# Optimization experiments

Measured on AMD Instinct MI355X. Metric: run time of the kernel, lower is better.

## Reference

```python
import jax, jax.numpy as jnp
import numpy as np

H = 4        # num_heads
KNN = 10     # k_knn neighbors gathered by distance
KS = 4       # k_select top-k neighbors kept by attention score
EPS = 1e-5
BIG = 1e9


def _ln(x, g, b):
    m = x.mean(-1, keepdims=True)
    v = ((x - m) ** 2).mean(-1, keepdims=True)
    return (x - m) * jax.lax.rsqrt(v + EPS) * g + b


def _sparse_dyn_voxel_attn(x, coords, mask, w_qkv, b_qkv, w_proj, b_proj):
    # x: [B,N,C], coords: [B,N,3], mask: [B,N] bool
    B, N, C = x.shape
    dh = C // H
    qkv = x @ w_qkv + b_qkv                       # [B,N,3C]
    q, k, v = jnp.split(qkv, 3, axis=-1)
    q = q.reshape(B, N, H, dh).transpose(0, 2, 1, 3)   # [B,H,N,dh]
    k = k.reshape(B, N, H, dh).transpose(0, 2, 1, 3)
    v = v.reshape(B, N, H, dh).transpose(0, 2, 1, 3)

    # KNN over voxel coordinates; empty voxels pushed to far distance
    d2 = jnp.sum((coords[:, :, None, :] - coords[:, None, :, :]) ** 2, axis=-1)  # [B,N,N]
    d2 = jnp.where(mask[:, None, :], d2, BIG)
    _, nbr = jax.lax.top_k(-d2, KNN)              # [B,N,KNN] nearest-neighbor indices

    # gather neighbor keys/values: [B,H,N,KNN,dh]
    kn = jax.vmap(lambda a, i: a[:, i, :])(k, nbr)
    vn = jax.vmap(lambda a, i: a[:, i, :])(v, nbr)
    nmask = jax.vmap(lambda m, i: m[i])(mask, nbr)  # [B,N,KNN]

    scale = float(1.0 / np.sqrt(dh))
    scores = jnp.einsum('bhnd,bhnkd->bhnk', q, kn) * scale  # [B,H,N,KNN]
    scores = scores + jnp.where(nmask, 0.0, -BIG)[:, None, :, :]

    # dynamic selection: keep top k_select neighbors by score, softmax over them
    sv, si = jax.lax.top_k(scores, KS)            # [B,H,N,KS]
    w = jax.nn.softmax(sv, axis=-1)
    vsel = jnp.take_along_axis(vn, si[..., None], axis=3)   # [B,H,N,KS,dh]
    o = jnp.einsum('bhnk,bhnkd->bhnd', w, vsel)   # [B,H,N,dh]
    o = o.transpose(0, 2, 1, 3).reshape(B, N, C) @ w_proj + b_proj
    return jnp.where(mask[..., None], o, 0.0)


def setup_inputs() -> dict:
    key = jax.random.key(0)
    ks = jax.random.split(key, 8)
    B, N, C, M = 4, 4096, 64, 256  # N = 16^3 voxels
    s = lambda k, sh: jax.random.normal(k, sh, jnp.float32) * 0.02
    return dict(
        inputs=jax.random.normal(ks[0], (B, N, C), jnp.float32),
        voxel_coords=jax.random.uniform(ks[1], (B, N, 3), jnp.float32) * 16.0,
        non_empty_mask=jax.random.randint(ks[2], (B, N), 0, 2).astype(bool),
        ln1_g=jnp.ones(C, jnp.float32), ln1_b=jnp.zeros(C, jnp.float32),
        ln2_g=jnp.ones(C, jnp.float32), ln2_b=jnp.zeros(C, jnp.float32),
        w_qkv=s(ks[3], (C, 3 * C)), b_qkv=jnp.zeros(3 * C, jnp.float32),
        w_proj=s(ks[4], (C, C)), b_proj=jnp.zeros(C, jnp.float32),
        w1=s(ks[5], (C, M)), b1=jnp.zeros(M, jnp.float32),
        w2=s(ks[6], (M, C)), b2=jnp.zeros(C, jnp.float32),
    )


def reference(inputs, voxel_coords, non_empty_mask, ln1_g, ln1_b, ln2_g, ln2_b,
              w_qkv, b_qkv, w_proj, b_proj, w1, b1, w2, b2):
    a = _sparse_dyn_voxel_attn(_ln(inputs, ln1_g, ln1_b), voxel_coords,
                               non_empty_mask, w_qkv, b_qkv, w_proj, b_proj)
    x = 0.5 * a + inputs                          # drop_path(attn)*0.5 + shortcut (eval)
    h = jax.nn.gelu(_ln(x, ln2_g, ln2_b) @ w1 + b1) @ w2 + b2
    return 0.5 * h + x
```

## Files before the change

### kernel.cpp

```cpp
#include <hip/hip_runtime.h>
#include <hip/hip_bf16.h>
#include <math.h>

#define NH   4
#define DH   16
#define CH   64
#define KNN  10
#define KS   4
#define NV   4096
#define NB   4
#define MHID 256
#define BN   (NB * NV)

#define P_LN1G  0
#define P_LN1B  64
#define P_LN2G  128
#define P_LN2B  192
#define P_WQKV  256
#define P_BQKV  12544
#define P_WPROJ 12736
#define P_BPROJ 16832
#define P_W1    16896
#define P_B1    33280
#define P_W2    33536
#define P_B2    49920
#define P_TOT   49984

#define N_ING  (BN * CH + NB * NV * 3 + P_TOT + BN)
#define N_PACK (16384 + 16384 + 12288)

typedef __hip_bfloat16 bf16;
typedef __attribute__((ext_vector_type(8))) short short8;
typedef __attribute__((ext_vector_type(4))) float float4a;

__device__ __forceinline__ float b2f(bf16 x) { return __bfloat162float(x); }

__device__ __forceinline__ float cvt(const void* p, int i, int isbf) {
  return isbf ? b2f(((const bf16*)p)[i]) : ((const float*)p)[i];
}

__device__ __forceinline__ float wave_sum_f32(float v) {
#pragma unroll
  for (int m = 32; m >= 1; m >>= 1) v += __shfl_xor(v, m, 64);
  return v;
}

__device__ __forceinline__ void wave_min_kv(unsigned& hi, unsigned& lo) {
#pragma unroll
  for (int m = 32; m >= 1; m >>= 1) {
    unsigned ohi = __shfl_xor(hi, m, 64);
    unsigned olo = __shfl_xor(lo, m, 64);
    if (ohi < hi || (ohi == hi && olo < lo)) { hi = ohi; lo = olo; }
  }
}

__device__ __forceinline__ float tanh_fast(float u) {
  float e = __expf(2.0f * u);
  return 1.0f - 2.0f / (e + 1.0f);
}

__device__ __forceinline__ float d2f(float x, float y, float z,
                                     float qx, float qy, float qz) {
  float dx = x - qx, dy = y - qy, dz = z - qz;
  return dx * dx + dy * dy + dz * dz;
}

__global__ __launch_bounds__(256) void k_prep(
    const void* xin, const void* coords, const void* maskr,
    const void* ln1g, const void* ln1b, const void* ln2g, const void* ln2b,
    const void* wqkv, const void* bqkv, const void* wproj, const void* bproj,
    const void* w1, const void* b1, const void* w2, const void* b2,
    float* __restrict__ xcan, float* __restrict__ ccan,
    float* __restrict__ pcan, int* __restrict__ mcan,
    unsigned short* __restrict__ w1p, unsigned short* __restrict__ w2p,
    unsigned short* __restrict__ wqp, int* __restrict__ flags)
{
  __shared__ int sfl[2];
  const int tid = threadIdx.x;
  if (tid < 64) {
    const unsigned short* xu = (const unsigned short*)xin;
    const unsigned* mu = (const unsigned*)maskr;
    int cnt = 0;
#pragma unroll
    for (int k = 0; k < 4; ++k) {
      unsigned short w = xu[tid * 4 + k];
      int e = (w >> 7) & 0xFF;
      cnt += (e >= 100 && e <= 140);
    }
#pragma unroll
    for (int m = 32; m >= 1; m >>= 1) cnt += __shfl_xor(cnt, m, 64);
    unsigned big = (mu[tid] > 1u) ? 1u : 0u;
#pragma unroll
    for (int m = 32; m >= 1; m >>= 1) big |= __shfl_xor(big, m, 64);
    if (tid == 0) {
      sfl[0] = (cnt >= 205) ? 1 : 0;
      sfl[1] = big ? 1 : 0;
      if (blockIdx.x == 0) { flags[0] = sfl[0]; flags[1] = sfl[1]; }
    }
  }
  __syncthreads();
  const int isbf = sfl[0], m8 = sfl[1];

  int id = blockIdx.x * 256 + tid;
  const int n0 = BN * CH, n1 = NB * NV * 3, n2 = P_TOT, n3 = BN;
  if (id < n0) { xcan[id] = cvt(xin, id, isbf); return; }
  id -= n0;
  if (id < n1) { ccan[id] = cvt(coords, id, isbf); return; }
  id -= n1;
  if (id < n2) {
    const void* src; int off;
    if      (id < P_LN1B)  { src = ln1g;  off = id - P_LN1G; }
    else if (id < P_LN2G)  { src = ln1b;  off = id - P_LN1B; }
    else if (id < P_LN2B)  { src = ln2g;  off = id - P_LN2G; }
    else if (id < P_WQKV)  { src = ln2b;  off = id - P_LN2B; }
    else if (id < P_BQKV)  { src = wqkv;  off = id - P_WQKV; }
    else if (id < P_WPROJ) { src = bqkv;  off = id - P_BQKV; }
    else if (id < P_BPROJ) { src = wproj; off = id - P_WPROJ; }
    else if (id < P_W1)    { src = bproj; off = id - P_BPROJ; }
    else if (id < P_B1)    { src = w1;    off = id - P_W1; }
    else if (id < P_W2)    { src = b1;    off = id - P_B1; }
    else if (id < P_B2)    { src = w2;    off = id - P_W2; }
    else                   { src = b2;    off = id - P_B2; }
    pcan[id] = cvt(src, off, isbf);
    return;
  }
  id -= n2;
  if (id < n3) {
    mcan[id] = m8 ? (int)(((const unsigned char*)maskr)[id] != 0)
                  : (int)(((const int*)maskr)[id] != 0);
    return;
  }
  id -= n3;
  if (id < 16384) {
    int j = id & 7, l = (id >> 3) & 63, kh = (id >> 9) & 1, nt = id >> 10;
    int k = kh * 32 + ((l >> 4) * 8) + j;
    int n = nt * 16 + (l & 15);
    w1p[id] = __bfloat16_as_ushort(__float2bfloat16(cvt(w1, k * MHID + n, isbf)));
    return;
  }
  id -= 16384;
  if (id < 16384) {
    int j = id & 7, l = (id >> 3) & 63, kh = (id >> 9) & 7, nt = id >> 12;
    int k = kh * 32 + ((l >> 4) * 8) + j;
    int n = nt * 16 + (l & 15);
    w2p[id] = __bfloat16_as_ushort(__float2bfloat16(cvt(w2, k * CH + n, isbf)));
    return;
  }
  id -= 16384;
  if (id < 12288) {
    int j = id & 7, l = (id >> 3) & 63, kh = (id >> 9) & 1, nt = id >> 10;
    int k = kh * 32 + ((l >> 4) * 8) + j;
    int n = nt * 16 + (l & 15);
    wqp[id] = __bfloat16_as_ushort(__float2bfloat16(cvt(wqkv, k * 192 + n, isbf)));
  }
}

#define XQS 72
__global__ __launch_bounds__(256) void k_ln_qkv(
    const float* __restrict__ x, const float* __restrict__ pcan,
    const unsigned short* __restrict__ wqp, float* __restrict__ qkv)
{
  __shared__ unsigned short xnb[16 * XQS];
  const int tid = threadIdx.x;
  const int wave = tid >> 6, lane = tid & 63;
  const int row0 = blockIdx.x * 16;

  {
    const float gg = pcan[P_LN1G + lane], bb = pcan[P_LN1B + lane];
#pragma unroll
    for (int r = 0; r < 4; ++r) {
      int m = wave * 4 + r;
      float v = x[(size_t)(row0 + m) * CH + lane];
      float mn = wave_sum_f32(v) * (1.0f / 64.0f);
      float d = v - mn;
      float var = wave_sum_f32(d * d) * (1.0f / 64.0f);
      float rs = 1.0f / sqrtf(var + 1e-5f);
      xnb[m * XQS + lane] =
          __bfloat16_as_ushort(__float2bfloat16(d * rs * gg + bb));
    }
  }
  __syncthreads();

  const int q = lane >> 4, c = lane & 15;
  short8 a0 = *(const short8*)&xnb[c * XQS + q * 8];
  short8 a1 = *(const short8*)&xnb[c * XQS + 32 + q * 8];

#pragma unroll
  for (int t = 0; t < 3; ++t) {
    int nt = wave * 3 + t;
    short8 b0 = *(const short8*)&wqp[(size_t)((nt * 2 + 0) * 64 + lane) * 8];
    short8 b1 = *(const short8*)&wqp[(size_t)((nt * 2 + 1) * 64 + lane) * 8];
    float4a z = {0.f, 0.f, 0.f, 0.f};
    z = __builtin_amdgcn_mfma_f32_16x16x32_bf16(a0, b0, z, 0, 0, 0);
    z = __builtin_amdgcn_mfma_f32_16x16x32_bf16(a1, b1, z, 0, 0, 0);
    int n = nt * 16 + c;
    float bq = pcan[P_BQKV + n];
#pragma unroll
    for (int r = 0; r < 4; ++r) {
      int m = q * 4 + r;
      qkv[(size_t)(row0 + m) * 192 + n] = z[r] + bq;
    }
  }
}

#define KROWS 4
#define CAP   128
__global__ __launch_bounds__(256) void k_knn(
    const float* __restrict__ ccan, const int* __restrict__ mcan,
    int* __restrict__ nbr)
{
  __shared__ float4 sx[NV / 4], sy[NV / 4], sz[NV / 4];
  __shared__ unsigned long long sbuf[KROWS][CAP];
  const int tid = threadIdx.x;
  const int row0 = blockIdx.x * KROWS;
  const int b = row0 >> 12;
  const float* cb = ccan + (size_t)b * NV * 3;
  const int* mb = mcan + b * NV;

  float* fx = (float*)sx; float* fy = (float*)sy; float* fz = (float*)sz;
  for (int j = tid; j < NV; j += 256) {
    bool v = mb[j] != 0;
    float x = cb[j * 3], y = cb[j * 3 + 1], z = cb[j * 3 + 2];
    fx[j] = v ? x : 1e4f;
    fy[j] = v ? y : 1e4f;
    fz[j] = v ? z : 1e4f;
  }
  __syncthreads();
  const int wave = tid >> 6, lane = tid & 63;
  const int qi = (row0 & (NV - 1)) + wave;
  const float qx = cb[qi * 3], qy = cb[qi * 3 + 1], qz = cb[qi * 3 + 2];

  float bmin = 1e30f;
#pragma unroll 4
  for (int t = 0; t < 16; ++t) {
    float4 X = sx[lane + t * 64], Y = sy[lane + t * 64], Z = sz[lane + t * 64];
    float d0 = d2f(X.x, Y.x, Z.x, qx, qy, qz);
    float d1 = d2f(X.y, Y.y, Z.y, qx, qy, qz);
    float d2 = d2f(X.z, Y.z, Z.z, qx, qy, qz);
    float d3 = d2f(X.w, Y.w, Z.w, qx, qy, qz);
    bmin = fminf(bmin, fminf(fminf(d0, d1), fminf(d2, d3)));
  }

  const unsigned lm = __float_as_uint(bmin);
  unsigned acc = 0;
#pragma unroll 1
  for (int bit = 31; bit >= 0; --bit) {
    unsigned tr = acc | (1u << bit);
    int cnt = __popcll(__ballot(lm < tr));
    if (cnt <= KNN - 1) acc = tr;
  }
  const float T = __uint_as_float(acc + 8);

  int base = 0;
  const unsigned long long below = (lane == 0) ? 0ull : (~0ull >> (64 - lane));
#pragma unroll 4
  for (int t = 0; t < 16; ++t) {
    float4 X = sx[lane + t * 64], Y = sy[lane + t * 64], Z = sz[lane + t * 64];
    float dd[4];
    dd[0] = d2f(X.x, Y.x, Z.x, qx, qy, qz);
    dd[1] = d2f(X.y, Y.y, Z.y, qx, qy, qz);
    dd[2] = d2f(X.z, Y.z, Z.z, qx, qy, qz);
    dd[3] = d2f(X.w, Y.w, Z.w, qx, qy, qz);
#pragma unroll
    for (int e = 0; e < 4; ++e) {
      bool s = (dd[e] <= T);
      unsigned long long bal = __ballot(s);
      if (bal) {
        int pos = base + __popcll(bal & below);
        unsigned j = 4u * (unsigned)(lane + t * 64) + (unsigned)e;
        if (s && pos < CAP)
          sbuf[wave][pos] =
              ((unsigned long long)__float_as_uint(dd[e]) << 32) | j;
        base += __popcll(bal);
      }
    }
  }
  const int c = base;
  const int grow = row0 + wave;

  if (c >= KNN && c <= CAP) {
#pragma unroll
    for (int o = 0; o < 2; ++o) {
      int idx = lane + o * 64;
      if (idx < c) {
        unsigned long long mykey = sbuf[wave][idx];
        int rank = 0;
        for (int i = 0; i < c; ++i) rank += (sbuf[wave][i] < mykey);
        if (rank < KNN)
          nbr[(size_t)grow * KNN + rank] = (int)(mykey & (NV - 1));
      }
    }
  } else {
    unsigned long long arr[KNN];
#pragma unroll
    for (int t = 0; t < KNN; ++t) arr[t] = ~0ull;
    for (int t = 0; t < 16; ++t) {
      float4 X = sx[lane + t * 64], Y = sy[lane + t * 64], Z = sz[lane + t * 64];
      float dd[4];
      dd[0] = d2f(X.x, Y.x, Z.x, qx, qy, qz);
      dd[1] = d2f(X.y, Y.y, Z.y, qx, qy, qz);
      dd[2] = d2f(X.z, Y.z, Z.z, qx, qy, qz);
      dd[3] = d2f(X.w, Y.w, Z.w, qx, qy, qz);
#pragma unroll
      for (int e = 0; e < 4; ++e) {
        unsigned j = 4u * (unsigned)(lane + t * 64) + (unsigned)e;
        unsigned long long key =
            ((unsigned long long)__float_as_uint(dd[e]) << 32) | j;
        if (key < arr[KNN - 1]) {
          arr[KNN - 1] = key;
#pragma unroll
          for (int t2 = KNN - 1; t2 > 0; --t2) {
            unsigned long long a = arr[t2 - 1], cc = arr[t2];
            if (cc < a) { arr[t2 - 1] = cc; arr[t2] = a; }
          }
        }
      }
    }
    unsigned myj = 0;
#pragma unroll 1
    for (int r = 0; r < KNN; ++r) {
      unsigned hi = (unsigned)(arr[0] >> 32);
      unsigned lo = (unsigned)(arr[0] & 0xffffffffu);
      wave_min_kv(hi, lo);
      if (lane == (int)((lo >> 2) & 63u)) {
#pragma unroll
        for (int t = 0; t < KNN - 1; ++t) arr[t] = arr[t + 1];
        arr[KNN - 1] = ~0ull;
      }
      if (lane == r) myj = lo;
    }
    if (lane < KNN) nbr[(size_t)grow * KNN + lane] = (int)(myj & (NV - 1));
  }
}

#define AROWS 4
__global__ __launch_bounds__(256) void k_attn(
    const float* __restrict__ qkv, const int* __restrict__ nbr,
    const int* __restrict__ mcan, const float* __restrict__ xcan,
    const float* __restrict__ pcan, float* __restrict__ xres)
{
  __shared__ float wp[CH * CH];
  __shared__ float bp[CH];
  __shared__ float sc[AROWS][NH][KNN];
  __shared__ float wsel[AROWS][NH][KS];
  __shared__ int   isel[AROWS][NH][KS];
  __shared__ float obuf[AROWS][CH];
  __shared__ int   nb[AROWS][KNN];
  __shared__ float npen[AROWS][KNN];
  const int tid = threadIdx.x;
  {
    const float4* src = (const float4*)(pcan + P_WPROJ);
    float4* dst = (float4*)wp;
    for (int i = tid; i < CH * CH / 4; i += 256) dst[i] = src[i];
    if (tid < CH) bp[tid] = pcan[P_BPROJ + tid];
  }
  const int wave = tid >> 6, lane = tid & 63;
  const int row = blockIdx.x * AROWS + wave;
  const int b = row / NV;

  if (lane < KNN) {
    int j = nbr[(size_t)row * KNN + lane] & (NV - 1);
    nb[wave][lane] = j;
    npen[wave][lane] = mcan[b * NV + j] ? 0.0f : -1e9f;
  }
  __syncthreads();

  if (lane < NH * KNN) {
    int h = lane / KNN, kk = lane % KNN;
    int j = nb[wave][kk];
    const float* qp = qkv + (size_t)row * 192 + h * DH;
    const float* kp = qkv + ((size_t)(b * NV + j)) * 192 + 64 + h * DH;
    float acc = 0.f;
#pragma unroll
    for (int d = 0; d < DH; ++d) acc += qp[d] * kp[d];
    sc[wave][h][kk] = acc * 0.25f + npen[wave][kk];
  }
  __syncthreads();

  if (lane < NH) {
    int h = lane;
    float sv[KS]; int sj[KS];
    unsigned used = 0;
#pragma unroll
    for (int r = 0; r < KS; ++r) {
      float best = -INFINITY; int bi = 0;
#pragma unroll
      for (int kk = 0; kk < KNN; ++kk) {
        float s = sc[wave][h][kk];
        if (!(used & (1u << kk)) && s > best) { best = s; bi = kk; }
      }
      used |= 1u << bi; sv[r] = best; sj[r] = bi;
    }
    float mx = sv[0];
    float e[KS], sum = 0.f;
#pragma unroll
    for (int r = 0; r < KS; ++r) { e[r] = expf(sv[r] - mx); sum += e[r]; }
    float inv = 1.0f / sum;
#pragma unroll
    for (int r = 0; r < KS; ++r) {
      wsel[wave][h][r] = e[r] * inv;
      isel[wave][h][r] = nb[wave][sj[r]];
    }
  }
  __syncthreads();

  {
    int h = lane >> 4, d = lane & 15;
    float o = 0.f;
#pragma unroll
    for (int r = 0; r < KS; ++r) {
      int j = isel[wave][h][r];
      o += wsel[wave][h][r] * qkv[((size_t)(b * NV + j)) * 192 + 128 + h * DH + d];
    }
    obuf[wave][lane] = o;
  }
  __syncthreads();

  {
    float acc = bp[lane];
#pragma unroll 4
    for (int cc = 0; cc < CH; ++cc)
      acc = fmaf(obuf[wave][cc], wp[cc * CH + lane], acc);
    float a = mcan[row] ? acc : 0.0f;
    xres[(size_t)row * CH + lane] = 0.5f * a + xcan[(size_t)row * CH + lane];
  }
}

#define XNS 72
#define GS  264
__global__ __launch_bounds__(256) void k_mlp(
    const float* __restrict__ xres, const float* __restrict__ pcan,
    const unsigned short* __restrict__ w1p,
    const unsigned short* __restrict__ w2p,
    const int* __restrict__ flags, void* __restrict__ out)
{
  __shared__ unsigned short xnb[16 * XNS];
  __shared__ unsigned short gb[16 * GS];
  const int tid = threadIdx.x;
  const int wave = tid >> 6, lane = tid & 63;
  const int row0 = blockIdx.x * 16;

  {
    const float gg = pcan[P_LN2G + lane], bb2 = pcan[P_LN2B + lane];
#pragma unroll
    for (int r = 0; r < 4; ++r) {
      int m = wave * 4 + r;
      float v = xres[(size_t)(row0 + m) * CH + lane];
      float mn = wave_sum_f32(v) * (1.0f / 64.0f);
      float d = v - mn;
      float var = wave_sum_f32(d * d) * (1.0f / 64.0f);
      float rs = 1.0f / sqrtf(var + 1e-5f);
      xnb[m * XNS + lane] =
          __bfloat16_as_ushort(__float2bfloat16(d * rs * gg + bb2));
    }
  }
  __syncthreads();

  const int q = lane >> 4, c = lane & 15;
  short8 a0 = *(const short8*)&xnb[c * XNS + q * 8];
  short8 a1 = *(const short8*)&xnb[c * XNS + 32 + q * 8];

  float4a acc[4];
#pragma unroll
  for (int t = 0; t < 4; ++t) {
    int nt = wave * 4 + t;
    short8 b0 = *(const short8*)&w1p[(size_t)((nt * 2 + 0) * 64 + lane) * 8];
    short8 b1 = *(const short8*)&w1p[(size_t)((nt * 2 + 1) * 64 + lane) * 8];
    float4a z = {0.f, 0.f, 0.f, 0.f};
    z = __builtin_amdgcn_mfma_f32_16x16x32_bf16(a0, b0, z, 0, 0, 0);
    z = __builtin_amdgcn_mfma_f32_16x16x32_bf16(a1, b1, z, 0, 0, 0);
    acc[t] = z;
  }
#pragma unroll
  for (int t = 0; t < 4; ++t) {
    int n = (wave * 4 + t) * 16 + c;
    float bo = pcan[P_B1 + n];
#pragma unroll
    for (int r = 0; r < 4; ++r) {
      float h = acc[t][r] + bo;
      float u = 0.7978845608028654f * (h + 0.044715f * h * h * h);
      float gv = 0.5f * h * (1.0f + tanh_fast(u));
      gb[(q * 4 + r) * GS + n] = __bfloat16_as_ushort(__float2bfloat16(gv));
    }
  }
  __syncthreads();

  float4a o = {0.f, 0.f, 0.f, 0.f};
#pragma unroll
  for (int kh = 0; kh < 8; ++kh) {
    short8 ag = *(const short8*)&gb[c * GS + kh * 32 + q * 8];
    short8 bg = *(const short8*)&w2p[(size_t)((wave * 8 + kh) * 64 + lane) * 8];
    o = __builtin_amdgcn_mfma_f32_16x16x32_bf16(ag, bg, o, 0, 0, 0);
  }
  {
    int n = wave * 16 + c;
    float b2v = pcan[P_B2 + n];
    const int isbf = flags[0];
#pragma unroll
    for (int r = 0; r < 4; ++r) {
      int m = q * 4 + r;
      size_t idx = (size_t)(row0 + m) * CH + n;
      float val = 0.5f * (o[r] + b2v) + xres[idx];
      if (isbf) ((bf16*)out)[idx] = __float2bfloat16(val);
      else      ((float*)out)[idx] = val;
    }
  }
}

extern "C" void kernel_launch(void* const* d_in, const int* in_sizes, int n_in,
                              void* d_out, int out_size, void* d_ws, size_t ws_size,
                              hipStream_t stream)
{
  char* ws = (char*)d_ws;
  float* qkv   = (float*)(ws);
  float* xres  = (float*)(ws + 12582912);
  float* xcan  = (float*)(ws + 16777216);
  float* ccan  = (float*)(ws + 20971520);
  float* pcan  = (float*)(ws + 21168128);
  int*   mcan  = (int*)  (ws + 21368064);
  int*   nbr   = (int*)  (ws + 21433600);
  int*   flags = (int*)  (ws + 22088960);
  unsigned short* w1p = (unsigned short*)(ws + 22089728);
  unsigned short* w2p = (unsigned short*)(ws + 22122496);
  unsigned short* wqp = (unsigned short*)(ws + 22155264);

  const int total = N_ING + N_PACK;
  k_prep<<<(total + 255) / 256, 256, 0, stream>>>(
      d_in[0], d_in[1], d_in[2], d_in[3], d_in[4], d_in[5], d_in[6],
      d_in[7], d_in[8], d_in[9], d_in[10], d_in[11], d_in[12], d_in[13], d_in[14],
      xcan, ccan, pcan, mcan, w1p, w2p, wqp, flags);
  k_ln_qkv<<<BN / 16, 256, 0, stream>>>(xcan, pcan, wqp, qkv);
  k_knn<<<BN / KROWS, 256, 0, stream>>>(ccan, mcan, nbr);
  k_attn<<<BN / AROWS, 256, 0, stream>>>(qkv, nbr, mcan, xcan, pcan, xres);
  k_mlp<<<BN / 16, 256, 0, stream>>>(xres, pcan, w1p, w2p, flags, d_out);
}
```

Before: 171.5 us.

## Replace brute-force KNN with uniform-grid binning and ring search

A new kernel counting-sorts the valid voxels of each batch into a 16^3 grid of cells, with a scan producing per-cell start offsets. A per-thread KNN kernel then searches expanding rings of cells around each valid query, keeping a sorted top-10 of (distance, index) keys. It stops once the 10th distance is within the ring radius. This replaces the O(N^2) all-pairs distance scan with a mostly local search. The attention kernel also skips its work for masked rows and just copies the residual. The cost is per-thread divergence and irregular, uncoalesced loads from binned points.

```diff
diff --git a/kernel.cpp b/kernel.cpp
--- a/kernel.cpp
+++ b/kernel.cpp
@@ -45,15 +45,6 @@
   return v;
 }
 
-__device__ __forceinline__ void wave_min_kv(unsigned& hi, unsigned& lo) {
-#pragma unroll
-  for (int m = 32; m >= 1; m >>= 1) {
-    unsigned ohi = __shfl_xor(hi, m, 64);
-    unsigned olo = __shfl_xor(lo, m, 64);
-    if (ohi < hi || (ohi == hi && olo < lo)) { hi = ohi; lo = olo; }
-  }
-}
-
 __device__ __forceinline__ float tanh_fast(float u) {
   float e = __expf(2.0f * u);
   return 1.0f - 2.0f / (e + 1.0f);
@@ -63,6 +54,21 @@
                                      float qx, float qy, float qz) {
   float dx = x - qx, dy = y - qy, dz = z - qz;
   return dx * dx + dy * dy + dz * dz;
+}
+
+__device__ __forceinline__ void knn_insert(unsigned long long* arr,
+                                           unsigned long long key) {
+  if (key < arr[KNN - 1]) {
+#pragma unroll
+    for (int t = 0; t < KNN; ++t) {
+      unsigned long long a = arr[t];
+      bool lt = key < a;
+      unsigned long long mn = lt ? key : a;
+      unsigned long long mx = lt ? a : key;
+      arr[t] = mn;
+      key = mx;
+    }
+  }
 }
 
 __global__ __launch_bounds__(256) void k_prep(
@@ -203,134 +209,150 @@
   }
 }
 
-#define KROWS 4
-#define CAP   128
-__global__ __launch_bounds__(256) void k_knn(
+__global__ __launch_bounds__(1024) void k_bin(
     const float* __restrict__ ccan, const int* __restrict__ mcan,
-    int* __restrict__ nbr)
-{
-  __shared__ float4 sx[NV / 4], sy[NV / 4], sz[NV / 4];
-  __shared__ unsigned long long sbuf[KROWS][CAP];
-  const int tid = threadIdx.x;
-  const int row0 = blockIdx.x * KROWS;
-  const int b = row0 >> 12;
+    float4* __restrict__ pbin, unsigned* __restrict__ bstart)
+{
+  __shared__ unsigned cnt[NV];
+  __shared__ unsigned woff[16];
+  const int b = blockIdx.x, tid = threadIdx.x;
   const float* cb = ccan + (size_t)b * NV * 3;
   const int* mb = mcan + b * NV;
-
-  float* fx = (float*)sx; float* fy = (float*)sy; float* fz = (float*)sz;
-  for (int j = tid; j < NV; j += 256) {
-    bool v = mb[j] != 0;
-    float x = cb[j * 3], y = cb[j * 3 + 1], z = cb[j * 3 + 2];
-    fx[j] = v ? x : 1e4f;
-    fy[j] = v ? y : 1e4f;
-    fz[j] = v ? z : 1e4f;
-  }
-  __syncthreads();
-  const int wave = tid >> 6, lane = tid & 63;
-  const int qi = (row0 & (NV - 1)) + wave;
-  const float qx = cb[qi * 3], qy = cb[qi * 3 + 1], qz = cb[qi * 3 + 2];
-
-  float bmin = 1e30f;
-#pragma unroll 4
-  for (int t = 0; t < 16; ++t) {
-    float4 X = sx[lane + t * 64], Y = sy[lane + t * 64], Z = sz[lane + t * 64];
-    float d0 = d2f(X.x, Y.x, Z.x, qx, qy, qz);
-    float d1 = d2f(X.y, Y.y, Z.y, qx, qy, qz);
-    float d2 = d2f(X.z, Y.z, Z.z, qx, qy, qz);
-    float d3 = d2f(X.w, Y.w, Z.w, qx, qy, qz);
-    bmin = fminf(bmin, fminf(fminf(d0, d1), fminf(d2, d3)));
-  }
-
-  const unsigned lm = __float_as_uint(bmin);
-  unsigned acc = 0;
-#pragma unroll 1
-  for (int bit = 31; bit >= 0; --bit) {
-    unsigned tr = acc | (1u << bit);
-    int cnt = __popcll(__ballot(lm < tr));
-    if (cnt <= KNN - 1) acc = tr;
-  }
-  const float T = __uint_as_float(acc + 8);
-
-  int base = 0;
-  const unsigned long long below = (lane == 0) ? 0ull : (~0ull >> (64 - lane));
-#pragma unroll 4
-  for (int t = 0; t < 16; ++t) {
-    float4 X = sx[lane + t * 64], Y = sy[lane + t * 64], Z = sz[lane + t * 64];
-    float dd[4];
-    dd[0] = d2f(X.x, Y.x, Z.x, qx, qy, qz);
-    dd[1] = d2f(X.y, Y.y, Z.y, qx, qy, qz);
-    dd[2] = d2f(X.z, Y.z, Z.z, qx, qy, qz);
-    dd[3] = d2f(X.w, Y.w, Z.w, qx, qy, qz);
-#pragma unroll
-    for (int e = 0; e < 4; ++e) {
-      bool s = (dd[e] <= T);
-      unsigned long long bal = __ballot(s);
-      if (bal) {
-        int pos = base + __popcll(bal & below);
-        unsigned j = 4u * (unsigned)(lane + t * 64) + (unsigned)e;
-        if (s && pos < CAP)
-          sbuf[wave][pos] =
-              ((unsigned long long)__float_as_uint(dd[e]) << 32) | j;
-        base += __popcll(bal);
-      }
-    }
-  }
-  const int c = base;
-  const int grow = row0 + wave;
-
-  if (c >= KNN && c <= CAP) {
-#pragma unroll
-    for (int o = 0; o < 2; ++o) {
-      int idx = lane + o * 64;
-      if (idx < c) {
-        unsigned long long mykey = sbuf[wave][idx];
-        int rank = 0;
-        for (int i = 0; i < c; ++i) rank += (sbuf[wave][i] < mykey);
-        if (rank < KNN)
-          nbr[(size_t)grow * KNN + rank] = (int)(mykey & (NV - 1));
-      }
-    }
-  } else {
-    unsigned long long arr[KNN];
-#pragma unroll
-    for (int t = 0; t < KNN; ++t) arr[t] = ~0ull;
-    for (int t = 0; t < 16; ++t) {
-      float4 X = sx[lane + t * 64], Y = sy[lane + t * 64], Z = sz[lane + t * 64];
-      float dd[4];
-      dd[0] = d2f(X.x, Y.x, Z.x, qx, qy, qz);
-      dd[1] = d2f(X.y, Y.y, Z.y, qx, qy, qz);
-      dd[2] = d2f(X.z, Y.z, Z.z, qx, qy, qz);
-      dd[3] = d2f(X.w, Y.w, Z.w, qx, qy, qz);
-#pragma unroll
-      for (int e = 0; e < 4; ++e) {
-        unsigned j = 4u * (unsigned)(lane + t * 64) + (unsigned)e;
-        unsigned long long key =
-            ((unsigned long long)__float_as_uint(dd[e]) << 32) | j;
-        if (key < arr[KNN - 1]) {
-          arr[KNN - 1] = key;
-#pragma unroll
-          for (int t2 = KNN - 1; t2 > 0; --t2) {
-            unsigned long long a = arr[t2 - 1], cc = arr[t2];
-            if (cc < a) { arr[t2 - 1] = cc; arr[t2] = a; }
+  unsigned* st = bstart + (size_t)b * 4104;
+
+#pragma unroll
+  for (int k = 0; k < 4; ++k) cnt[tid + k * 1024] = 0;
+  __syncthreads();
+
+#pragma unroll
+  for (int k = 0; k < 4; ++k) {
+    int j = tid + k * 1024;
+    if (mb[j]) {
+      int cx = (int)cb[j * 3];     cx = cx > 15 ? 15 : cx;
+      int cy = (int)cb[j * 3 + 1]; cy = cy > 15 ? 15 : cy;
+      int cz = (int)cb[j * 3 + 2]; cz = cz > 15 ? 15 : cz;
+      atomicAdd(&cnt[(cz << 8) + (cy << 4) + cx], 1u);
+    }
+  }
+  __syncthreads();
+
+  unsigned s0 = cnt[tid * 4], s1 = cnt[tid * 4 + 1];
+  unsigned s2 = cnt[tid * 4 + 2], s3 = cnt[tid * 4 + 3];
+  unsigned tot = s0 + s1 + s2 + s3;
+  unsigned v = tot;
+  const int wv = tid >> 6, ln = tid & 63;
+#pragma unroll
+  for (int d = 1; d < 64; d <<= 1) {
+    unsigned o = __shfl_up(v, d, 64);
+    if (ln >= d) v += o;
+  }
+  if (ln == 63) woff[wv] = v;
+  __syncthreads();
+  unsigned wpre = 0;
+  for (int w = 0; w < wv; ++w) wpre += woff[w];
+  unsigned r = wpre + v - tot;
+  cnt[tid * 4]     = r; st[tid * 4]     = r; r += s0;
+  cnt[tid * 4 + 1] = r; st[tid * 4 + 1] = r; r += s1;
+  cnt[tid * 4 + 2] = r; st[tid * 4 + 2] = r; r += s2;
+  cnt[tid * 4 + 3] = r; st[tid * 4 + 3] = r; r += s3;
+  if (tid == 1023) st[4096] = r;
+  __syncthreads();
+
+#pragma unroll
+  for (int k = 0; k < 4; ++k) {
+    int j = tid + k * 1024;
+    if (mb[j]) {
+      float x = cb[j * 3], y = cb[j * 3 + 1], z = cb[j * 3 + 2];
+      int cx = (int)x; cx = cx > 15 ? 15 : cx;
+      int cy = (int)y; cy = cy > 15 ? 15 : cy;
+      int cz = (int)z; cz = cz > 15 ? 15 : cz;
+      unsigned pos = atomicAdd(&cnt[(cz << 8) + (cy << 4) + cx], 1u);
+      float4 q; q.x = x; q.y = y; q.z = z; q.w = __int_as_float(j);
+      pbin[(size_t)b * NV + pos] = q;
+    }
+  }
+}
+
+__global__ __launch_bounds__(256) void k_knn2(
+    const float4* __restrict__ pbin, const unsigned* __restrict__ bstart,
+    int* __restrict__ nbr)
+{
+  const int g = blockIdx.x * 256 + threadIdx.x;
+  const int b = g >> 12, slot = g & (NV - 1);
+  const unsigned* st = bstart + (size_t)b * 4104;
+  const int nval = (int)st[4096];
+  if (slot >= nval) return;
+  const float4* pb = pbin + (size_t)b * NV;
+  float4 me = pb[slot];
+  const float qx = me.x, qy = me.y, qz = me.z;
+  const int qi = __float_as_int(me.w);
+  int cx = (int)qx; cx = cx > 15 ? 15 : cx;
+  int cy = (int)qy; cy = cy > 15 ? 15 : cy;
+  int cz = (int)qz; cz = cz > 15 ? 15 : cz;
+
+  unsigned long long arr[KNN];
+#pragma unroll
+  for (int t = 0; t < KNN; ++t) arr[t] = ~0ull;
+
+  for (int R = 0; R < 16; ++R) {
+    const int zlo = cz - R, zhi = cz + R;
+    const int z0 = zlo < 0 ? 0 : zlo, z1 = zhi > 15 ? 15 : zhi;
+    for (int z = z0; z <= z1; ++z) {
+      const bool zed = (z == zlo) || (z == zhi);
+      const int ylo = cy - R, yhi = cy + R;
+      const int y0 = ylo < 0 ? 0 : ylo, y1 = yhi > 15 ? 15 : yhi;
+      for (int y = y0; y <= y1; ++y) {
+        const bool yed = (y == ylo) || (y == yhi);
+        const int base = (z << 8) + (y << 4);
+        if (zed || yed) {
+          const int xa = (cx - R) < 0 ? 0 : (cx - R);
+          const int xb = (cx + R) > 15 ? 15 : (cx + R);
+          const int s = (int)st[base + xa], e = (int)st[base + xb + 1];
+          for (int i = s; i < e; ++i) {
+            float4 p = pb[i];
+            float d2 = d2f(p.x, p.y, p.z, qx, qy, qz);
+            unsigned long long key =
+                ((unsigned long long)__float_as_uint(d2) << 32) |
+                (unsigned)__float_as_int(p.w);
+            knn_insert(arr, key);
+          }
+        } else {
+          const int xl = cx - R, xr = cx + R;
+          if (xl >= 0) {
+            const int s = (int)st[base + xl], e = (int)st[base + xl + 1];
+            for (int i = s; i < e; ++i) {
+              float4 p = pb[i];
+              float d2 = d2f(p.x, p.y, p.z, qx, qy, qz);
+              unsigned long long key =
+                  ((unsigned long long)__float_as_uint(d2) << 32) |
+                  (unsigned)__float_as_int(p.w);
+              knn_insert(arr, key);
+            }
+          }
+          if (xr <= 15) {
+            const int s = (int)st[base + xr], e = (int)st[base + xr + 1];
+            for (int i = s; i < e; ++i) {
+              float4 p = pb[i];
+              float d2 = d2f(p.x, p.y, p.z, qx, qy, qz);
+              unsigned long long key =
+                  ((unsigned long long)__float_as_uint(d2) << 32) |
+                  (unsigned)__float_as_int(p.w);
+              knn_insert(arr, key);
+            }
           }
         }
       }
     }
-    unsigned myj = 0;
-#pragma unroll 1
-    for (int r = 0; r < KNN; ++r) {
-      unsigned hi = (unsigned)(arr[0] >> 32);
-      unsigned lo = (unsigned)(arr[0] & 0xffffffffu);
-      wave_min_kv(hi, lo);
-      if (lane == (int)((lo >> 2) & 63u)) {
-#pragma unroll
-        for (int t = 0; t < KNN - 1; ++t) arr[t] = arr[t + 1];
-        arr[KNN - 1] = ~0ull;
-      }
-      if (lane == r) myj = lo;
-    }
-    if (lane < KNN) nbr[(size_t)grow * KNN + lane] = (int)(myj & (NV - 1));
-  }
+    if (arr[KNN - 1] != ~0ull) {
+      float dk = __uint_as_float((unsigned)(arr[KNN - 1] >> 32));
+      if (dk <= (float)(R * R)) break;
+    }
+  }
+
+  const int row = (b << 12) | qi;
+#pragma unroll
+  for (int t = 0; t < KNN; ++t)
+    nbr[(size_t)row * KNN + t] = (int)(arr[t] & (NV - 1));
 }
 
 #define AROWS 4
@@ -357,15 +379,16 @@
   const int wave = tid >> 6, lane = tid & 63;
   const int row = blockIdx.x * AROWS + wave;
   const int b = row / NV;
-
-  if (lane < KNN) {
+  const bool live = mcan[row] != 0;
+
+  if (live && lane < KNN) {
     int j = nbr[(size_t)row * KNN + lane] & (NV - 1);
     nb[wave][lane] = j;
     npen[wave][lane] = mcan[b * NV + j] ? 0.0f : -1e9f;
   }
   __syncthreads();
 
-  if (lane < NH * KNN) {
+  if (live && lane < NH * KNN) {
     int h = lane / KNN, kk = lane % KNN;
     int j = nb[wave][kk];
     const float* qp = qkv + (size_t)row * 192 + h * DH;
@@ -377,7 +400,7 @@
   }
   __syncthreads();
 
-  if (lane < NH) {
+  if (live && lane < NH) {
     int h = lane;
     float sv[KS]; int sj[KS];
     unsigned used = 0;
@@ -404,7 +427,7 @@
   }
   __syncthreads();
 
-  {
+  if (live) {
     int h = lane >> 4, d = lane & 15;
     float o = 0.f;
 #pragma unroll
@@ -416,13 +439,14 @@
   }
   __syncthreads();
 
-  {
+  if (live) {
     float acc = bp[lane];
 #pragma unroll 4
     for (int cc = 0; cc < CH; ++cc)
       acc = fmaf(obuf[wave][cc], wp[cc * CH + lane], acc);
-    float a = mcan[row] ? acc : 0.0f;
-    xres[(size_t)row * CH + lane] = 0.5f * a + xcan[(size_t)row * CH + lane];
+    xres[(size_t)row * CH + lane] = 0.5f * acc + xcan[(size_t)row * CH + lane];
+  } else {
+    xres[(size_t)row * CH + lane] = xcan[(size_t)row * CH + lane];
   }
 }
 
@@ -523,14 +547,17 @@
   unsigned short* w1p = (unsigned short*)(ws + 22089728);
   unsigned short* w2p = (unsigned short*)(ws + 22122496);
   unsigned short* wqp = (unsigned short*)(ws + 22155264);
+  float4*   pbin   = (float4*)  (ws + 22179840);
+  unsigned* bstart = (unsigned*)(ws + 22441984);
 
   const int total = N_ING + N_PACK;
   k_prep<<<(total + 255) / 256, 256, 0, stream>>>(
       d_in[0], d_in[1], d_in[2], d_in[3], d_in[4], d_in[5], d_in[6],
       d_in[7], d_in[8], d_in[9], d_in[10], d_in[11], d_in[12], d_in[13], d_in[14],
       xcan, ccan, pcan, mcan, w1p, w2p, wqp, flags);
+  k_bin<<<NB, 1024, 0, stream>>>(ccan, mcan, pbin, bstart);
   k_ln_qkv<<<BN / 16, 256, 0, stream>>>(xcan, pcan, wqp, qkv);
-  k_knn<<<BN / KROWS, 256, 0, stream>>>(ccan, mcan, nbr);
+  k_knn2<<<BN / 256, 256, 0, stream>>>(pbin, bstart, nbr);
   k_attn<<<BN / AROWS, 256, 0, stream>>>(qkv, nbr, mcan, xcan, pcan, xres);
   k_mlp<<<BN / 16, 256, 0, stream>>>(xres, pcan, w1p, w2p, flags, d_out);
 }
```

New measurement: 239.6 us. 39.6% more time.
